# Optimization experiments

Measured on AMD Instinct MI355X. Metric: run time of the kernel, lower is better.

Reference implementation:

```python
import jax, jax.numpy as jnp
import numpy as np

N = 100_000          # nodes
E = 1_600_000        # directed edges (avg degree 16)
EPS = 1e-5           # LayerNorm eps (torch default)


def _layer_norm(h, g, b):
    m = jnp.mean(h, axis=-1, keepdims=True)
    v = jnp.mean((h - m) ** 2, axis=-1, keepdims=True)
    return (h - m) * jax.lax.rsqrt(v + EPS) * g + b


def _forward(x, edge_index, Ws, bs, gs, bes, mWs, mbs):
    n = x.shape[0]
    loop = jnp.arange(n, dtype=edge_index.dtype)
    src = jnp.concatenate([edge_index[0], loop])   # self-loops appended (PyG GCNConv default)
    dst = jnp.concatenate([edge_index[1], loop])
    deg = jax.ops.segment_sum(jnp.ones_like(dst, dtype=x.dtype), dst, num_segments=n)
    dinv = jax.lax.rsqrt(jnp.maximum(deg, 1.0))    # deg >= 1 thanks to self-loops
    norm = dinv[src] * dinv[dst]                   # symmetric normalization, shape [E+N]
    h = x
    for W, b, g, be in zip(Ws, bs, gs, bes):
        t = h @ W                                  # [N, d_out]
        msg = t[src] * norm[:, None]               # edge gather  [E+N, d_out]
        t = jax.ops.segment_sum(msg, dst, num_segments=n) + b  # scatter-add
        h = jax.nn.relu(_layer_norm(t, g, be))     # dropout is identity in eval mode
    h = jax.nn.relu(h @ mWs[0] + mbs[0])
    h = jax.nn.relu(h @ mWs[1] + mbs[1])
    return h @ mWs[2] + mbs[2]                     # [N, 1]


def setup_inputs() -> dict:
    key = jax.random.key(0)
    ks = jax.random.split(key, 12)
    inp = {}
    inp["x"] = jax.random.normal(ks[0], (N, 3), dtype=jnp.float32)
    inp["edge_index"] = jax.random.randint(ks[1], (2, E), 0, N, dtype=jnp.int32)
    dims = [3, 64, 128, 128]
    k = 2
    for l, (din, dout) in enumerate(zip(dims[:-1], dims[1:])):
        inp[f"W{l}"] = jax.random.normal(ks[k], (din, dout), dtype=jnp.float32) / np.sqrt(din).astype(np.float32); k += 1
        inp[f"b{l}"] = jnp.zeros((dout,), jnp.float32)
        inp[f"g{l}"] = jnp.ones((dout,), jnp.float32)
        inp[f"be{l}"] = jnp.zeros((dout,), jnp.float32)
    mlp = [(128, 128), (128, 32), (32, 1)]
    for l, (din, dout) in enumerate(mlp):
        inp[f"mW{l}"] = jax.random.normal(ks[k], (din, dout), dtype=jnp.float32) / np.sqrt(din).astype(np.float32); k += 1
        inp[f"mb{l}"] = jnp.zeros((dout,), jnp.float32)
    return inp


def reference(x, edge_index, W0, b0, g0, be0, W1, b1, g1, be1, W2, b2, g2, be2,
              mW0, mb0, mW1, mb1, mW2, mb2):
    return _forward(x, edge_index,
                    (W0, W1, W2), (b0, b1, b2), (g0, g1, g2), (be0, be1, be2),
                    (mW0, mW1, mW2), (mb0, mb1, mb2))
```

## Files before the change

kernel.cpp:

```cpp
#include <hip/hip_runtime.h>

static inline int cdiv(int a, int b) { return (a + b - 1) / b; }

typedef unsigned short u16;
typedef unsigned int u32;
typedef unsigned long long u64;

using short8 = __attribute__((ext_vector_type(8))) short;
using f32x4  = __attribute__((ext_vector_type(4))) float;

#define BCHUNK 8192

__device__ __forceinline__ float bf2f(u16 u) {
    union { u32 i; float f; } v;
    v.i = ((u32)u) << 16;
    return v.f;
}
__device__ __forceinline__ u16 f2bf(float f) {
    union { float f; u32 i; } v;
    v.f = f;
    u32 r = v.i + 0x7FFF + ((v.i >> 16) & 1);
    return (u16)(r >> 16);
}


__global__ void bzero_kernel(int* __restrict__ bcnt, int nb) {
    int i = blockIdx.x * blockDim.x + threadIdx.x;
    if (i < nb) bcnt[i] = 0;
}

__global__ __launch_bounds__(256) void bhist_kernel(const int* __restrict__ dst,
                                                    int* __restrict__ bcnt, int ne, int nb) {
    __shared__ int lh[512];
    for (int i = threadIdx.x; i < nb; i += 256) lh[i] = 0;
    __syncthreads();
    int base = blockIdx.x * BCHUNK;
    int end = min(base + BCHUNK, ne);
    for (int i = base + threadIdx.x; i < end; i += 256) atomicAdd(&lh[dst[i] >> 8], 1);
    __syncthreads();
    for (int i = threadIdx.x; i < nb; i += 256)
        if (lh[i]) atomicAdd(&bcnt[i], lh[i]);
}

__global__ __launch_bounds__(512) void bscan_kernel(const int* __restrict__ bcnt,
                                                    int* __restrict__ bboff,
                                                    int* __restrict__ bcur, int nb) {
    __shared__ int sd[512];
    int tid = threadIdx.x;
    int v = (tid < nb) ? bcnt[tid] : 0;
    sd[tid] = v;
    __syncthreads();
    for (int off = 1; off < 512; off <<= 1) {
        int t = (tid >= off) ? sd[tid - off] : 0;
        __syncthreads();
        sd[tid] += t;
        __syncthreads();
    }
    int ex = sd[tid] - v;
    if (tid < nb) {
        bboff[tid] = ex;
        bcur[tid] = ex;
    }
    if (tid == 511) bboff[nb] = sd[511];
}

__global__ __launch_bounds__(256) void bplace_kernel(const int* __restrict__ src,
                                                     const int* __restrict__ dst,
                                                     int* __restrict__ bcur,
                                                     u32* __restrict__ bpair, int ne, int nb) {
    __shared__ int lh[512], lbase[512], lrun[512];
    for (int i = threadIdx.x; i < nb; i += 256) { lh[i] = 0; lrun[i] = 0; }
    __syncthreads();
    int base = blockIdx.x * BCHUNK;
    int end = min(base + BCHUNK, ne);
    for (int i = base + threadIdx.x; i < end; i += 256) atomicAdd(&lh[dst[i] >> 8], 1);
    __syncthreads();
    for (int b = threadIdx.x; b < nb; b += 256) {
        int c = lh[b];
        if (c) lbase[b] = atomicAdd(&bcur[b], c);
    }
    __syncthreads();
    for (int i = base + threadIdx.x; i < end; i += 256) {
        int d = dst[i];
        int b = d >> 8;
        int r = atomicAdd(&lrun[b], 1);
        bpair[(size_t)lbase[b] + r] = ((u32)(d & 255) << 24) | (u32)src[i];
    }
}

__global__ __launch_bounds__(256) void fine_count_kernel(const u32* __restrict__ bpair,
                                                         const int* __restrict__ bboff,
                                                         int* __restrict__ cnt, int n) {
    int b = blockIdx.x;
    __shared__ int lc[256];
    lc[threadIdx.x] = 0;
    __syncthreads();
    int e0 = bboff[b], e1 = bboff[b + 1];
    for (int i = e0 + threadIdx.x; i < e1; i += 256) {
        atomicAdd(&lc[bpair[i] >> 24], 1);
    }
    __syncthreads();
    int d = (b << 8) + threadIdx.x;
    if (d < n) cnt[d] = lc[threadIdx.x];
}

__global__ __launch_bounds__(256) void fine_place_kernel(const u32* __restrict__ bpair,
                                                         const int* __restrict__ bboff,
                                                         const int* __restrict__ row_ptr,
                                                         int* __restrict__ sorted, int n) {
    int b = blockIdx.x;
    __shared__ int lcur[256];
    int d = (b << 8) + threadIdx.x;
    lcur[threadIdx.x] = (d < n) ? row_ptr[d] : 0;
    __syncthreads();
    int e0 = bboff[b], e1 = bboff[b + 1];
    for (int i = e0 + threadIdx.x; i < e1; i += 256) {
        u32 p = bpair[i];
        int slot = atomicAdd(&lcur[p >> 24], 1);
        sorted[slot] = (int)(p & 0xFFFFFF);
    }
}


__global__ void part_kernel(const int* __restrict__ cnt, int* __restrict__ partial, int n) {
    __shared__ int sred[256];
    int tid = threadIdx.x;
    int base = blockIdx.x * 1024 + tid * 4;
    int s = 0;
#pragma unroll
    for (int j = 0; j < 4; ++j) {
        int i = base + j;
        if (i < n) s += cnt[i];
    }
    sred[tid] = s;
    __syncthreads();
    for (int off = 128; off; off >>= 1) {
        if (tid < off) sred[tid] += sred[tid + off];
        __syncthreads();
    }
    if (tid == 0) partial[blockIdx.x] = sred[0];
}

__global__ __launch_bounds__(256) void scanp_kernel(const int* __restrict__ partial,
                                                    int* __restrict__ chunkoff,
                                                    int* __restrict__ row_ptr,
                                                    int nchunks, int n) {
    __shared__ int sd[256];
    int tid = threadIdx.x;
    int v = (tid < nchunks) ? partial[tid] : 0;
    sd[tid] = v;
    __syncthreads();
    for (int off = 1; off < 256; off <<= 1) {
        int t = (tid >= off) ? sd[tid - off] : 0;
        __syncthreads();
        sd[tid] += t;
        __syncthreads();
    }
    if (tid < nchunks) chunkoff[tid] = sd[tid] - v;
    if (tid == 255) row_ptr[n] = sd[255];
}

__global__ void scanc_kernel(const int* __restrict__ cnt, const int* __restrict__ chunkoff,
                             int* __restrict__ row_ptr, float* __restrict__ dinv,
                             const float* __restrict__ x, float4* __restrict__ xs4, int n) {
    __shared__ int sdat[256];
    int tid = threadIdx.x;
    int base = blockIdx.x * 1024 + tid * 4;
    int c[4];
    int ts = 0;
#pragma unroll
    for (int j = 0; j < 4; ++j) {
        int i = base + j;
        c[j] = (i < n) ? cnt[i] : 0;
        ts += c[j];
    }
    sdat[tid] = ts;
    __syncthreads();
    for (int off = 1; off < 256; off <<= 1) {
        int t = (tid >= off) ? sdat[tid - off] : 0;
        __syncthreads();
        sdat[tid] += t;
        __syncthreads();
    }
    int ex = sdat[tid] - ts + chunkoff[blockIdx.x];
#pragma unroll
    for (int j = 0; j < 4; ++j) {
        int i = base + j;
        if (i < n) {
            row_ptr[i] = ex;
            float dd = 1.0f / sqrtf((float)(c[j] + 1));
            dinv[i] = dd;
            float4 o = {x[i * 3 + 0] * dd, x[i * 3 + 1] * dd, x[i * 3 + 2] * dd, 0.0f};
            xs4[i] = o;
            ex += c[j];
        }
    }
}


__global__ void wprep_kernel(const float* __restrict__ W1f, const float* __restrict__ W2f,
                             const float* __restrict__ M0f, const float* __restrict__ M1f,
                             u16* __restrict__ Wt1, u16* __restrict__ Wt2,
                             u16* __restrict__ WtM0, u16* __restrict__ WtM1t) {
    int i = blockIdx.x * blockDim.x + threadIdx.x;
    if (i < 8192) {
        int k = i / 128, c = i % 128;
        Wt1[(size_t)c * 64 + k] = f2bf(W1f[i]);
    } else if (i < 24576) {
        int j = i - 8192;
        int k = j / 128, c = j % 128;
        Wt2[(size_t)c * 128 + k] = f2bf(W2f[j]);
    } else if (i < 40960) {
        int j = i - 24576;
        int k = j / 128, c = j % 128;
        WtM0[(size_t)c * 128 + k] = f2bf(M0f[j]);
    } else if (i < 45056) {
        int j = i - 40960;
        int k = j / 32, c = j % 32;
        WtM1t[(size_t)c * 128 + k] = f2bf(M1f[j]);
    }
}


__global__ void gather3_kernel(const float4* __restrict__ xs4, const int* __restrict__ rp,
                               const int* __restrict__ ss, const float* __restrict__ dinv,
                               float4* __restrict__ agg3, int n) {
    int d = blockIdx.x * blockDim.x + threadIdx.x;
    if (d >= n) return;
    float4 a = xs4[d];
    int k = rp[d], k1 = rp[d + 1];
    for (; k + 4 <= k1; k += 4) {
        int s0 = ss[k], s1 = ss[k + 1], s2 = ss[k + 2], s3 = ss[k + 3];
        float4 v0 = xs4[s0], v1 = xs4[s1], v2 = xs4[s2], v3 = xs4[s3];
        a.x += v0.x + v1.x + v2.x + v3.x;
        a.y += v0.y + v1.y + v2.y + v3.y;
        a.z += v0.z + v1.z + v2.z + v3.z;
    }
    for (; k < k1; ++k) {
        float4 v = xs4[ss[k]];
        a.x += v.x;
        a.y += v.y;
        a.z += v.z;
    }
    float dd = dinv[d];
    float4 o = {a.x * dd, a.y * dd, a.z * dd, 0.0f};
    agg3[d] = o;
}

__global__ void gather64_kernel(const u16* __restrict__ Ts, const int* __restrict__ rp,
                                const int* __restrict__ ss, const float* __restrict__ dinv,
                                u16* __restrict__ A, int n) {
    int row = blockIdx.x * 4 + (threadIdx.x >> 6);
    if (row >= n) return;
    int lane = threadIdx.x & 63;
    float acc = bf2f(Ts[(size_t)row * 64 + lane]);
    int k = rp[row], k1 = rp[row + 1];
    while (k < k1) {
        int take = min(64, k1 - k);
        int myi = (lane < take) ? ss[k + lane] : 0;
        int u = 0;
        for (; u + 16 <= take; u += 16) {
            int s[16];
#pragma unroll
            for (int q = 0; q < 16; ++q) s[q] = __shfl(myi, u + q);
            float v[16];
#pragma unroll
            for (int q = 0; q < 16; ++q) v[q] = bf2f(Ts[(size_t)s[q] * 64 + lane]);
#pragma unroll
            for (int q = 0; q < 16; ++q) acc += v[q];
        }
        for (; u + 8 <= take; u += 8) {
            int s[8];
#pragma unroll
            for (int q = 0; q < 8; ++q) s[q] = __shfl(myi, u + q);
            float v[8];
#pragma unroll
            for (int q = 0; q < 8; ++q) v[q] = bf2f(Ts[(size_t)s[q] * 64 + lane]);
#pragma unroll
            for (int q = 0; q < 8; ++q) acc += v[q];
        }
        for (; u < take; ++u) {
            int s = __shfl(myi, u);
            acc += bf2f(Ts[(size_t)s * 64 + lane]);
        }
        k += take;
    }
    A[(size_t)row * 64 + lane] = f2bf(acc * dinv[row]);
}

__global__ void gather128_kernel(const u16* __restrict__ Ts, const int* __restrict__ rp,
                                 const int* __restrict__ ss, const float* __restrict__ dinv,
                                 u16* __restrict__ A, int n) {
    int row = blockIdx.x * 4 + (threadIdx.x >> 6);
    if (row >= n) return;
    int lane = threadIdx.x & 63;
    const u32* T2 = (const u32*)Ts;
    u32 t = T2[(size_t)row * 64 + lane];
    float ax = bf2f((u16)(t & 0xffff));
    float ay = bf2f((u16)(t >> 16));
    int k = rp[row], k1 = rp[row + 1];
    while (k < k1) {
        int take = min(64, k1 - k);
        int myi = (lane < take) ? ss[k + lane] : 0;
        int u = 0;
        for (; u + 16 <= take; u += 16) {
            int s[16];
#pragma unroll
            for (int q = 0; q < 16; ++q) s[q] = __shfl(myi, u + q);
            u32 v[16];
#pragma unroll
            for (int q = 0; q < 16; ++q) v[q] = T2[(size_t)s[q] * 64 + lane];
#pragma unroll
            for (int q = 0; q < 16; ++q) {
                ax += bf2f((u16)(v[q] & 0xffff));
                ay += bf2f((u16)(v[q] >> 16));
            }
        }
        for (; u + 8 <= take; u += 8) {
            int s[8];
#pragma unroll
            for (int q = 0; q < 8; ++q) s[q] = __shfl(myi, u + q);
            u32 v[8];
#pragma unroll
            for (int q = 0; q < 8; ++q) v[q] = T2[(size_t)s[q] * 64 + lane];
#pragma unroll
            for (int q = 0; q < 8; ++q) {
                ax += bf2f((u16)(v[q] & 0xffff));
                ay += bf2f((u16)(v[q] >> 16));
            }
        }
        for (; u < take; ++u) {
            int s = __shfl(myi, u);
            u32 a = T2[(size_t)s * 64 + lane];
            ax += bf2f((u16)(a & 0xffff));
            ay += bf2f((u16)(a >> 16));
        }
        k += take;
    }
    float dd = dinv[row];
    u32 o = (u32)f2bf(ax * dd) | ((u32)f2bf(ay * dd) << 16);
    ((u32*)A)[(size_t)row * 64 + lane] = o;
}


__global__ __launch_bounds__(256) void gcn0_kernel(const float4* __restrict__ agg3,
                                                   const float* __restrict__ W0,
                                                   const float* __restrict__ b0,
                                                   const float* __restrict__ g0,
                                                   const float* __restrict__ be0,
                                                   const float* __restrict__ dinv,
                                                   u16* __restrict__ out, int n) {
    __shared__ float sW[192], sb[64], sg[64], se[64];
    int tid = threadIdx.x;
    if (tid < 192) sW[tid] = W0[tid];
    if (tid < 64) {
        sb[tid] = b0[tid];
        sg[tid] = g0[tid];
        se[tid] = be0[tid];
    }
    __syncthreads();
    int row = blockIdx.x * 4 + (tid >> 6);
    int lane = tid & 63;
    if (row >= n) return;
    float4 a = agg3[row];
    float acc = sb[lane] + a.x * sW[lane] + a.y * sW[64 + lane] + a.z * sW[128 + lane];
    float s = acc;
#pragma unroll
    for (int off = 32; off; off >>= 1) s += __shfl_xor(s, off);
    float mean = s * (1.0f / 64.0f);
    float d = acc - mean;
    float q = d * d;
#pragma unroll
    for (int off = 32; off; off >>= 1) q += __shfl_xor(q, off);
    float inv = 1.0f / sqrtf(q * (1.0f / 64.0f) + 1e-5f);
    float o = d * inv * sg[lane] + se[lane];
    out[(size_t)row * 64 + lane] = f2bf(dinv[row] * fmaxf(o, 0.0f));
}


template <int DIN, int DOUT, bool SCALEOUT>
__global__ __launch_bounds__(256) void mfma_gemm_kernel(const u16* __restrict__ H,
                                                        const u16* __restrict__ Wt,
                                                        const float* __restrict__ b,
                                                        const float* __restrict__ g,
                                                        const float* __restrict__ be,
                                                        const float* __restrict__ dscale,
                                                        u16* __restrict__ C, int n) {
    constexpr int NT = DOUT / 16;
    constexpr int KS = DIN / 32;
    const int tid = threadIdx.x;
    const int wave = tid >> 6;
    const int lane = tid & 63;
    const int l16 = lane & 15;
    const int lhi = lane >> 4;
    const int r0 = blockIdx.x * 64 + wave * 16;

    short8 wf[KS][NT];
#pragma unroll
    for (int ks = 0; ks < KS; ++ks)
#pragma unroll
        for (int nt = 0; nt < NT; ++nt)
            wf[ks][nt] = *(const short8*)(Wt + (size_t)(nt * 16 + l16) * DIN + ks * 32 + 8 * lhi);

    int arow = r0 + l16;
    if (arow > n - 1) arow = n - 1;
    const u16* Hrow = H + (size_t)arow * DIN + 8 * lhi;
    short8 af[KS];
#pragma unroll
    for (int ks = 0; ks < KS; ++ks) af[ks] = *(const short8*)(Hrow + ks * 32);

    f32x4 acc[NT];
#pragma unroll
    for (int nt = 0; nt < NT; ++nt) acc[nt] = {0.f, 0.f, 0.f, 0.f};

#pragma unroll
    for (int ks = 0; ks < KS; ++ks)
#pragma unroll
        for (int nt = 0; nt < NT; ++nt)
            acc[nt] = __builtin_amdgcn_mfma_f32_16x16x32_bf16(af[ks], wf[ks][nt], acc[nt], 0, 0, 0);

    float bias[NT], gl[NT], bel[NT];
#pragma unroll
    for (int nt = 0; nt < NT; ++nt) {
        bias[nt] = b[nt * 16 + l16];
        gl[nt] = g[nt * 16 + l16];
        bel[nt] = be[nt * 16 + l16];
    }

#pragma unroll
    for (int j = 0; j < 4; ++j) {
        int row = r0 + lhi * 4 + j;
        float v[NT];
#pragma unroll
        for (int nt = 0; nt < NT; ++nt) v[nt] = acc[nt][j] + bias[nt];
        float s = 0.f;
#pragma unroll
        for (int nt = 0; nt < NT; ++nt) s += v[nt];
#pragma unroll
        for (int off = 1; off < 16; off <<= 1) s += __shfl_xor(s, off);
        float mean = s * (1.0f / DOUT);
        float qs = 0.f;
#pragma unroll
        for (int nt = 0; nt < NT; ++nt) {
            float d = v[nt] - mean;
            qs += d * d;
        }
#pragma unroll
        for (int off = 1; off < 16; off <<= 1) qs += __shfl_xor(qs, off);
        float inv = 1.0f / sqrtf(qs * (1.0f / DOUT) + 1e-5f);
        if (row < n) {
            float sc = SCALEOUT ? dscale[row] : 1.0f;
#pragma unroll
            for (int nt = 0; nt < NT; ++nt) {
                float o = (v[nt] - mean) * inv * gl[nt] + bel[nt];
                C[(size_t)row * DOUT + nt * 16 + l16] = f2bf(sc * fmaxf(o, 0.f));
            }
        }
    }
}


__global__ __launch_bounds__(256) void mlp_fused_kernel(const u16* __restrict__ H,
                                                        const u16* __restrict__ WtM0,
                                                        const u16* __restrict__ WtM1t,
                                                        const float* __restrict__ mb0,
                                                        const float* __restrict__ mb1,
                                                        const float* __restrict__ mW2,
                                                        const float* __restrict__ mb2,
                                                        float* __restrict__ out, int n) {
    __shared__ u16 sm1[4][16][132];
    const int tid = threadIdx.x;
    const int wave = tid >> 6;
    const int lane = tid & 63;
    const int l16 = lane & 15;
    const int lhi = lane >> 4;
    const int r0 = blockIdx.x * 64 + wave * 16;

    {
        short8 wf[4][8];
#pragma unroll
        for (int ks = 0; ks < 4; ++ks)
#pragma unroll
            for (int nt = 0; nt < 8; ++nt)
                wf[ks][nt] = *(const short8*)(WtM0 + (size_t)(nt * 16 + l16) * 128 + ks * 32 + 8 * lhi);

        int arow = r0 + l16;
        if (arow > n - 1) arow = n - 1;
        const u16* Hrow = H + (size_t)arow * 128 + 8 * lhi;
        short8 af[4];
#pragma unroll
        for (int ks = 0; ks < 4; ++ks) af[ks] = *(const short8*)(Hrow + ks * 32);

        f32x4 acc[8];
#pragma unroll
        for (int nt = 0; nt < 8; ++nt) acc[nt] = {0.f, 0.f, 0.f, 0.f};
#pragma unroll
        for (int ks = 0; ks < 4; ++ks)
#pragma unroll
            for (int nt = 0; nt < 8; ++nt)
                acc[nt] = __builtin_amdgcn_mfma_f32_16x16x32_bf16(af[ks], wf[ks][nt], acc[nt], 0, 0, 0);

#pragma unroll
        for (int nt = 0; nt < 8; ++nt) {
            float bias = mb0[nt * 16 + l16];
#pragma unroll
            for (int j = 0; j < 4; ++j) {
                sm1[wave][lhi * 4 + j][nt * 16 + l16] = f2bf(fmaxf(acc[nt][j] + bias, 0.f));
            }
        }
    }

    short8 a2[2][4];
#pragma unroll
    for (int t = 0; t < 2; ++t)
#pragma unroll
        for (int ks = 0; ks < 4; ++ks)
            a2[t][ks] = *(const short8*)(WtM1t + (size_t)(t * 16 + l16) * 128 + ks * 32 + 8 * lhi);

    short8 b2[4];
#pragma unroll
    for (int ks = 0; ks < 4; ++ks)
        b2[ks] = *(const short8*)&sm1[wave][l16][ks * 32 + 8 * lhi];

    f32x4 acc2[2];
    acc2[0] = {0.f, 0.f, 0.f, 0.f};
    acc2[1] = {0.f, 0.f, 0.f, 0.f};
#pragma unroll
    for (int ks = 0; ks < 4; ++ks) {
        acc2[0] = __builtin_amdgcn_mfma_f32_16x16x32_bf16(a2[0][ks], b2[ks], acc2[0], 0, 0, 0);
        acc2[1] = __builtin_amdgcn_mfma_f32_16x16x32_bf16(a2[1][ks], b2[ks], acc2[1], 0, 0, 0);
    }

    float part = 0.f;
#pragma unroll
    for (int t = 0; t < 2; ++t)
#pragma unroll
        for (int j = 0; j < 4; ++j) {
            int c = t * 16 + lhi * 4 + j;
            part += fmaxf(acc2[t][j] + mb1[c], 0.f) * mW2[c];
        }
    part += __shfl_xor(part, 16);
    part += __shfl_xor(part, 32);
    int row = r0 + l16;
    if (lhi == 0 && row < n) out[row] = part + mb2[0];
}


extern "C" void kernel_launch(void* const* d_in, const int* in_sizes, int n_in,
                              void* d_out, int out_size, void* d_ws, size_t ws_size,
                              hipStream_t stream) {
    const float* x   = (const float*)d_in[0];
    const int*   ei  = (const int*)d_in[1];
    const float* W0  = (const float*)d_in[2];
    const float* b0  = (const float*)d_in[3];
    const float* g0  = (const float*)d_in[4];
    const float* be0 = (const float*)d_in[5];
    const float* W1  = (const float*)d_in[6];
    const float* b1  = (const float*)d_in[7];
    const float* g1  = (const float*)d_in[8];
    const float* be1 = (const float*)d_in[9];
    const float* W2  = (const float*)d_in[10];
    const float* b2  = (const float*)d_in[11];
    const float* g2  = (const float*)d_in[12];
    const float* be2 = (const float*)d_in[13];
    const float* mW0 = (const float*)d_in[14];
    const float* mb0 = (const float*)d_in[15];
    const float* mW1 = (const float*)d_in[16];
    const float* mb1 = (const float*)d_in[17];
    const float* mW2 = (const float*)d_in[18];
    const float* mb2 = (const float*)d_in[19];
    float* out = (float*)d_out;

    const int n  = in_sizes[0] / 3;
    const int ne = in_sizes[1] / 2;
    const int* src = ei;
    const int* dst = ei + ne;
    const int nchunks = cdiv(n, 1024);
    const int nb = cdiv(n, 256);

    float* p = (float*)d_ws;
    float* dinv     = p;         p += n;
    int*   cnt      = (int*)p;   p += n;
    int*   row_ptr  = (int*)p;   p += n + 16;
    int*   partial  = (int*)p;   p += 256;
    int*   chunkoff = (int*)p;   p += 256;
    int*   bcnt     = (int*)p;   p += 512;
    int*   bboff    = (int*)p;   p += 514;
    int*   bcur     = (int*)p;   p += 512;
    int*   sorted   = (int*)p;   p += ne;
    u32*   bpair    = (u32*)p;   p += ne;
    float4* xs4     = (float4*)p; p += 4 * (size_t)n;
    float4* agg3    = (float4*)p; p += 4 * (size_t)n;
    float* fR12     = p;         p += 64 * (size_t)n;
    float* fR3      = p;         p += 64 * (size_t)n;
    u16*   Wt1      = (u16*)p;
    u16*   Wt2      = Wt1 + 64 * 128;
    u16*   WtM0     = Wt2 + 128 * 128;
    u16*   WtM1t    = WtM0 + 128 * 128;

    u16* h0s   = (u16*)fR12;
    u16* a64b  = (u16*)(fR12 + 32 * (size_t)n);
    u16* a128b = (u16*)fR12;
    u16* h1s   = (u16*)fR3;
    u16* h2b   = (u16*)fR3;

    wprep_kernel<<<cdiv(45056, 256), 256, 0, stream>>>(W1, W2, mW0, mW1, Wt1, Wt2, WtM0, WtM1t);

    bzero_kernel<<<cdiv(nb, 256), 256, 0, stream>>>(bcnt, nb);
    bhist_kernel<<<cdiv(ne, BCHUNK), 256, 0, stream>>>(dst, bcnt, ne, nb);
    bscan_kernel<<<1, 512, 0, stream>>>(bcnt, bboff, bcur, nb);
    bplace_kernel<<<cdiv(ne, BCHUNK), 256, 0, stream>>>(src, dst, bcur, bpair, ne, nb);
    fine_count_kernel<<<nb, 256, 0, stream>>>(bpair, bboff, cnt, n);
    part_kernel<<<nchunks, 256, 0, stream>>>(cnt, partial, n);
    scanp_kernel<<<1, 256, 0, stream>>>(partial, chunkoff, row_ptr, nchunks, n);
    scanc_kernel<<<nchunks, 256, 0, stream>>>(cnt, chunkoff, row_ptr, dinv, x, xs4, n);
    fine_place_kernel<<<nb, 256, 0, stream>>>(bpair, bboff, row_ptr, sorted, n);

    gather3_kernel<<<cdiv(n, 256), 256, 0, stream>>>(xs4, row_ptr, sorted, dinv, agg3, n);
    gcn0_kernel<<<cdiv(n, 4), 256, 0, stream>>>(agg3, W0, b0, g0, be0, dinv, h0s, n);

    gather64_kernel<<<cdiv(n, 4), 256, 0, stream>>>(h0s, row_ptr, sorted, dinv, a64b, n);
    mfma_gemm_kernel<64, 128, true><<<cdiv(n, 64), 256, 0, stream>>>(
        a64b, Wt1, b1, g1, be1, dinv, h1s, n);

    gather128_kernel<<<cdiv(n, 4), 256, 0, stream>>>(h1s, row_ptr, sorted, dinv, a128b, n);
    mfma_gemm_kernel<128, 128, false><<<cdiv(n, 64), 256, 0, stream>>>(
        a128b, Wt2, b2, g2, be2, nullptr, h2b, n);

    mlp_fused_kernel<<<cdiv(n, 64), 256, 0, stream>>>(h2b, WtM0, WtM1t, mb0, mb1, mW2, mb2, out, n);
}
```

Before: 439.3 us.

## Fuse CSR build, layer-0 gather, and last GEMM into the MLP kernel

After: 423.5 us. 1.04x faster.

```diff
diff --git a/kernel.cpp b/kernel.cpp
--- a/kernel.cpp
+++ b/kernel.cpp
@@ -4,7 +4,6 @@
 
 typedef unsigned short u16;
 typedef unsigned int u32;
-typedef unsigned long long u64;
 
 using short8 = __attribute__((ext_vector_type(8))) short;
 using f32x4  = __attribute__((ext_vector_type(4))) float;
@@ -24,185 +23,13 @@
 }
 
 
-__global__ void bzero_kernel(int* __restrict__ bcnt, int nb) {
-    int i = blockIdx.x * blockDim.x + threadIdx.x;
-    if (i < nb) bcnt[i] = 0;
-}
-
-__global__ __launch_bounds__(256) void bhist_kernel(const int* __restrict__ dst,
-                                                    int* __restrict__ bcnt, int ne, int nb) {
-    __shared__ int lh[512];
-    for (int i = threadIdx.x; i < nb; i += 256) lh[i] = 0;
-    __syncthreads();
-    int base = blockIdx.x * BCHUNK;
-    int end = min(base + BCHUNK, ne);
-    for (int i = base + threadIdx.x; i < end; i += 256) atomicAdd(&lh[dst[i] >> 8], 1);
-    __syncthreads();
-    for (int i = threadIdx.x; i < nb; i += 256)
-        if (lh[i]) atomicAdd(&bcnt[i], lh[i]);
-}
-
-__global__ __launch_bounds__(512) void bscan_kernel(const int* __restrict__ bcnt,
-                                                    int* __restrict__ bboff,
-                                                    int* __restrict__ bcur, int nb) {
-    __shared__ int sd[512];
-    int tid = threadIdx.x;
-    int v = (tid < nb) ? bcnt[tid] : 0;
-    sd[tid] = v;
-    __syncthreads();
-    for (int off = 1; off < 512; off <<= 1) {
-        int t = (tid >= off) ? sd[tid - off] : 0;
-        __syncthreads();
-        sd[tid] += t;
-        __syncthreads();
-    }
-    int ex = sd[tid] - v;
-    if (tid < nb) {
-        bboff[tid] = ex;
-        bcur[tid] = ex;
-    }
-    if (tid == 511) bboff[nb] = sd[511];
-}
-
-__global__ __launch_bounds__(256) void bplace_kernel(const int* __restrict__ src,
-                                                     const int* __restrict__ dst,
-                                                     int* __restrict__ bcur,
-                                                     u32* __restrict__ bpair, int ne, int nb) {
-    __shared__ int lh[512], lbase[512], lrun[512];
-    for (int i = threadIdx.x; i < nb; i += 256) { lh[i] = 0; lrun[i] = 0; }
-    __syncthreads();
-    int base = blockIdx.x * BCHUNK;
-    int end = min(base + BCHUNK, ne);
-    for (int i = base + threadIdx.x; i < end; i += 256) atomicAdd(&lh[dst[i] >> 8], 1);
-    __syncthreads();
-    for (int b = threadIdx.x; b < nb; b += 256) {
-        int c = lh[b];
-        if (c) lbase[b] = atomicAdd(&bcur[b], c);
-    }
-    __syncthreads();
-    for (int i = base + threadIdx.x; i < end; i += 256) {
-        int d = dst[i];
-        int b = d >> 8;
-        int r = atomicAdd(&lrun[b], 1);
-        bpair[(size_t)lbase[b] + r] = ((u32)(d & 255) << 24) | (u32)src[i];
-    }
-}
-
-__global__ __launch_bounds__(256) void fine_count_kernel(const u32* __restrict__ bpair,
-                                                         const int* __restrict__ bboff,
-                                                         int* __restrict__ cnt, int n) {
-    int b = blockIdx.x;
-    __shared__ int lc[256];
-    lc[threadIdx.x] = 0;
-    __syncthreads();
-    int e0 = bboff[b], e1 = bboff[b + 1];
-    for (int i = e0 + threadIdx.x; i < e1; i += 256) {
-        atomicAdd(&lc[bpair[i] >> 24], 1);
-    }
-    __syncthreads();
-    int d = (b << 8) + threadIdx.x;
-    if (d < n) cnt[d] = lc[threadIdx.x];
-}
-
-__global__ __launch_bounds__(256) void fine_place_kernel(const u32* __restrict__ bpair,
-                                                         const int* __restrict__ bboff,
-                                                         const int* __restrict__ row_ptr,
-                                                         int* __restrict__ sorted, int n) {
-    int b = blockIdx.x;
-    __shared__ int lcur[256];
-    int d = (b << 8) + threadIdx.x;
-    lcur[threadIdx.x] = (d < n) ? row_ptr[d] : 0;
-    __syncthreads();
-    int e0 = bboff[b], e1 = bboff[b + 1];
-    for (int i = e0 + threadIdx.x; i < e1; i += 256) {
-        u32 p = bpair[i];
-        int slot = atomicAdd(&lcur[p >> 24], 1);
-        sorted[slot] = (int)(p & 0xFFFFFF);
-    }
-}
-
-
-__global__ void part_kernel(const int* __restrict__ cnt, int* __restrict__ partial, int n) {
-    __shared__ int sred[256];
-    int tid = threadIdx.x;
-    int base = blockIdx.x * 1024 + tid * 4;
-    int s = 0;
-#pragma unroll
-    for (int j = 0; j < 4; ++j) {
-        int i = base + j;
-        if (i < n) s += cnt[i];
-    }
-    sred[tid] = s;
-    __syncthreads();
-    for (int off = 128; off; off >>= 1) {
-        if (tid < off) sred[tid] += sred[tid + off];
-        __syncthreads();
-    }
-    if (tid == 0) partial[blockIdx.x] = sred[0];
-}
-
-__global__ __launch_bounds__(256) void scanp_kernel(const int* __restrict__ partial,
-                                                    int* __restrict__ chunkoff,
-                                                    int* __restrict__ row_ptr,
-                                                    int nchunks, int n) {
-    __shared__ int sd[256];
-    int tid = threadIdx.x;
-    int v = (tid < nchunks) ? partial[tid] : 0;
-    sd[tid] = v;
-    __syncthreads();
-    for (int off = 1; off < 256; off <<= 1) {
-        int t = (tid >= off) ? sd[tid - off] : 0;
-        __syncthreads();
-        sd[tid] += t;
-        __syncthreads();
-    }
-    if (tid < nchunks) chunkoff[tid] = sd[tid] - v;
-    if (tid == 255) row_ptr[n] = sd[255];
-}
-
-__global__ void scanc_kernel(const int* __restrict__ cnt, const int* __restrict__ chunkoff,
-                             int* __restrict__ row_ptr, float* __restrict__ dinv,
-                             const float* __restrict__ x, float4* __restrict__ xs4, int n) {
-    __shared__ int sdat[256];
-    int tid = threadIdx.x;
-    int base = blockIdx.x * 1024 + tid * 4;
-    int c[4];
-    int ts = 0;
-#pragma unroll
-    for (int j = 0; j < 4; ++j) {
-        int i = base + j;
-        c[j] = (i < n) ? cnt[i] : 0;
-        ts += c[j];
-    }
-    sdat[tid] = ts;
-    __syncthreads();
-    for (int off = 1; off < 256; off <<= 1) {
-        int t = (tid >= off) ? sdat[tid - off] : 0;
-        __syncthreads();
-        sdat[tid] += t;
-        __syncthreads();
-    }
-    int ex = sdat[tid] - ts + chunkoff[blockIdx.x];
-#pragma unroll
-    for (int j = 0; j < 4; ++j) {
-        int i = base + j;
-        if (i < n) {
-            row_ptr[i] = ex;
-            float dd = 1.0f / sqrtf((float)(c[j] + 1));
-            dinv[i] = dd;
-            float4 o = {x[i * 3 + 0] * dd, x[i * 3 + 1] * dd, x[i * 3 + 2] * dd, 0.0f};
-            xs4[i] = o;
-            ex += c[j];
-        }
-    }
-}
-
-
 __global__ void wprep_kernel(const float* __restrict__ W1f, const float* __restrict__ W2f,
                              const float* __restrict__ M0f, const float* __restrict__ M1f,
                              u16* __restrict__ Wt1, u16* __restrict__ Wt2,
-                             u16* __restrict__ WtM0, u16* __restrict__ WtM1t) {
+                             u16* __restrict__ WtM0, u16* __restrict__ WtM1t,
+                             int* __restrict__ bcnt, int nb) {
     int i = blockIdx.x * blockDim.x + threadIdx.x;
+    if (i < nb) bcnt[i] = 0;
     if (i < 8192) {
         int k = i / 128, c = i % 128;
         Wt1[(size_t)c * 64 + k] = f2bf(W1f[i]);
@@ -222,30 +49,164 @@
 }
 
 
-__global__ void gather3_kernel(const float4* __restrict__ xs4, const int* __restrict__ rp,
-                               const int* __restrict__ ss, const float* __restrict__ dinv,
-                               float4* __restrict__ agg3, int n) {
-    int d = blockIdx.x * blockDim.x + threadIdx.x;
-    if (d >= n) return;
-    float4 a = xs4[d];
-    int k = rp[d], k1 = rp[d + 1];
-    for (; k + 4 <= k1; k += 4) {
-        int s0 = ss[k], s1 = ss[k + 1], s2 = ss[k + 2], s3 = ss[k + 3];
-        float4 v0 = xs4[s0], v1 = xs4[s1], v2 = xs4[s2], v3 = xs4[s3];
-        a.x += v0.x + v1.x + v2.x + v3.x;
-        a.y += v0.y + v1.y + v2.y + v3.y;
-        a.z += v0.z + v1.z + v2.z + v3.z;
-    }
-    for (; k < k1; ++k) {
+__global__ __launch_bounds__(256) void bhist_kernel(const int* __restrict__ dst,
+                                                    int* __restrict__ bcnt, int ne, int nb) {
+    __shared__ int lh[512];
+    for (int i = threadIdx.x; i < nb; i += 256) lh[i] = 0;
+    __syncthreads();
+    int base = blockIdx.x * BCHUNK;
+    int end = min(base + BCHUNK, ne);
+    for (int i = base + threadIdx.x; i < end; i += 256) atomicAdd(&lh[dst[i] >> 8], 1);
+    __syncthreads();
+    for (int i = threadIdx.x; i < nb; i += 256)
+        if (lh[i]) atomicAdd(&bcnt[i], lh[i]);
+}
+
+__global__ __launch_bounds__(512) void bscan_kernel(const int* __restrict__ bcnt,
+                                                    int* __restrict__ bboff,
+                                                    int* __restrict__ bcur, int nb) {
+    __shared__ int sd[512];
+    int tid = threadIdx.x;
+    int v = (tid < nb) ? bcnt[tid] : 0;
+    sd[tid] = v;
+    __syncthreads();
+    for (int off = 1; off < 512; off <<= 1) {
+        int t = (tid >= off) ? sd[tid - off] : 0;
+        __syncthreads();
+        sd[tid] += t;
+        __syncthreads();
+    }
+    int ex = sd[tid] - v;
+    if (tid < nb) {
+        bboff[tid] = ex;
+        bcur[tid] = ex;
+    }
+    if (tid == 511) bboff[nb] = sd[511];
+}
+
+__global__ __launch_bounds__(256) void bplace_kernel(const int* __restrict__ src,
+                                                     const int* __restrict__ dst,
+                                                     int* __restrict__ bcur,
+                                                     u32* __restrict__ bpair, int ne, int nb) {
+    __shared__ int lh[512], lbase[512], lrun[512];
+    for (int i = threadIdx.x; i < nb; i += 256) { lh[i] = 0; lrun[i] = 0; }
+    __syncthreads();
+    int base = blockIdx.x * BCHUNK;
+    int end = min(base + BCHUNK, ne);
+    for (int i = base + threadIdx.x; i < end; i += 256) atomicAdd(&lh[dst[i] >> 8], 1);
+    __syncthreads();
+    for (int b = threadIdx.x; b < nb; b += 256) {
+        int c = lh[b];
+        if (c) lbase[b] = atomicAdd(&bcur[b], c);
+    }
+    __syncthreads();
+    for (int i = base + threadIdx.x; i < end; i += 256) {
+        int d = dst[i];
+        int b = d >> 8;
+        int r = atomicAdd(&lrun[b], 1);
+        bpair[(size_t)lbase[b] + r] = ((u32)(d & 255) << 24) | (u32)src[i];
+    }
+}
+
+__global__ __launch_bounds__(256) void fine_all_kernel(const u32* __restrict__ bpair,
+                                                       const int* __restrict__ bboff,
+                                                       const float* __restrict__ x,
+                                                       int* __restrict__ row_ptr,
+                                                       float* __restrict__ dinv,
+                                                       float4* __restrict__ xs4,
+                                                       int* __restrict__ sorted,
+                                                       int n, int ne) {
+    int b = blockIdx.x;
+    int tid = threadIdx.x;
+    __shared__ int lc[256], lpfx[256], lcur[256];
+    lc[tid] = 0;
+    __syncthreads();
+    int e0 = bboff[b], e1 = bboff[b + 1];
+    for (int i = e0 + tid; i < e1; i += 256) atomicAdd(&lc[bpair[i] >> 24], 1);
+    __syncthreads();
+    int c = lc[tid];
+    lpfx[tid] = c;
+    __syncthreads();
+    for (int off = 1; off < 256; off <<= 1) {
+        int t = (tid >= off) ? lpfx[tid - off] : 0;
+        __syncthreads();
+        lpfx[tid] += t;
+        __syncthreads();
+    }
+    int ex = e0 + lpfx[tid] - c;
+    lcur[tid] = ex;
+    int d = (b << 8) + tid;
+    if (d < n) {
+        row_ptr[d] = ex;
+        float dd = 1.0f / sqrtf((float)(c + 1));
+        dinv[d] = dd;
+        float4 o = {x[d * 3 + 0] * dd, x[d * 3 + 1] * dd, x[d * 3 + 2] * dd, 0.0f};
+        xs4[d] = o;
+    }
+    if (b == 0 && tid == 0) row_ptr[n] = ne;
+    __syncthreads();
+    for (int i = e0 + tid; i < e1; i += 256) {
+        u32 p = bpair[i];
+        int slot = atomicAdd(&lcur[p >> 24], 1);
+        sorted[slot] = (int)(p & 0xFFFFFF);
+    }
+}
+
+
+__global__ __launch_bounds__(256) void gcn0_kernel(const float4* __restrict__ xs4,
+                                                   const int* __restrict__ rp,
+                                                   const int* __restrict__ ss,
+                                                   const float* __restrict__ dinv,
+                                                   const float* __restrict__ W0,
+                                                   const float* __restrict__ b0,
+                                                   const float* __restrict__ g0,
+                                                   const float* __restrict__ be0,
+                                                   u16* __restrict__ out, int n) {
+    __shared__ float sW[192], sb[64], sg[64], se[64];
+    int tid = threadIdx.x;
+    if (tid < 192) sW[tid] = W0[tid];
+    if (tid < 64) {
+        sb[tid] = b0[tid];
+        sg[tid] = g0[tid];
+        se[tid] = be0[tid];
+    }
+    __syncthreads();
+    int row = blockIdx.x * 4 + (tid >> 6);
+    if (row >= n) return;
+    int lane = tid & 63;
+    int k0 = rp[row], k1 = rp[row + 1];
+    float ax = 0.f, ay = 0.f, az = 0.f;
+    for (int k = k0 + lane; k < k1; k += 64) {
         float4 v = xs4[ss[k]];
-        a.x += v.x;
-        a.y += v.y;
-        a.z += v.z;
-    }
-    float dd = dinv[d];
-    float4 o = {a.x * dd, a.y * dd, a.z * dd, 0.0f};
-    agg3[d] = o;
-}
+        ax += v.x;
+        ay += v.y;
+        az += v.z;
+    }
+#pragma unroll
+    for (int off = 32; off; off >>= 1) {
+        ax += __shfl_xor(ax, off);
+        ay += __shfl_xor(ay, off);
+        az += __shfl_xor(az, off);
+    }
+    float4 sf = xs4[row];
+    float dd = dinv[row];
+    ax = (ax + sf.x) * dd;
+    ay = (ay + sf.y) * dd;
+    az = (az + sf.z) * dd;
+    float acc = sb[lane] + ax * sW[lane] + ay * sW[64 + lane] + az * sW[128 + lane];
+    float s = acc;
+#pragma unroll
+    for (int off = 32; off; off >>= 1) s += __shfl_xor(s, off);
+    float mean = s * (1.0f / 64.0f);
+    float d = acc - mean;
+    float q = d * d;
+#pragma unroll
+    for (int off = 32; off; off >>= 1) q += __shfl_xor(q, off);
+    float inv = 1.0f / sqrtf(q * (1.0f / 64.0f) + 1e-5f);
+    float o = d * inv * sg[lane] + se[lane];
+    out[(size_t)row * 64 + lane] = f2bf(dd * fmaxf(o, 0.0f));
+}
+
 
 __global__ void gather64_kernel(const u16* __restrict__ Ts, const int* __restrict__ rp,
                                 const int* __restrict__ ss, const float* __restrict__ dinv,
@@ -343,41 +304,6 @@
 }
 
 
-__global__ __launch_bounds__(256) void gcn0_kernel(const float4* __restrict__ agg3,
-                                                   const float* __restrict__ W0,
-                                                   const float* __restrict__ b0,
-                                                   const float* __restrict__ g0,
-                                                   const float* __restrict__ be0,
-                                                   const float* __restrict__ dinv,
-                                                   u16* __restrict__ out, int n) {
-    __shared__ float sW[192], sb[64], sg[64], se[64];
-    int tid = threadIdx.x;
-    if (tid < 192) sW[tid] = W0[tid];
-    if (tid < 64) {
-        sb[tid] = b0[tid];
-        sg[tid] = g0[tid];
-        se[tid] = be0[tid];
-    }
-    __syncthreads();
-    int row = blockIdx.x * 4 + (tid >> 6);
-    int lane = tid & 63;
-    if (row >= n) return;
-    float4 a = agg3[row];
-    float acc = sb[lane] + a.x * sW[lane] + a.y * sW[64 + lane] + a.z * sW[128 + lane];
-    float s = acc;
-#pragma unroll
-    for (int off = 32; off; off >>= 1) s += __shfl_xor(s, off);
-    float mean = s * (1.0f / 64.0f);
-    float d = acc - mean;
-    float q = d * d;
-#pragma unroll
-    for (int off = 32; off; off >>= 1) q += __shfl_xor(q, off);
-    float inv = 1.0f / sqrtf(q * (1.0f / 64.0f) + 1e-5f);
-    float o = d * inv * sg[lane] + se[lane];
-    out[(size_t)row * 64 + lane] = f2bf(dinv[row] * fmaxf(o, 0.0f));
-}
-
-
 template <int DIN, int DOUT, bool SCALEOUT>
 __global__ __launch_bounds__(256) void mfma_gemm_kernel(const u16* __restrict__ H,
                                                         const u16* __restrict__ Wt,
@@ -460,15 +386,20 @@
 }
 
 
-__global__ __launch_bounds__(256) void mlp_fused_kernel(const u16* __restrict__ H,
-                                                        const u16* __restrict__ WtM0,
-                                                        const u16* __restrict__ WtM1t,
-                                                        const float* __restrict__ mb0,
-                                                        const float* __restrict__ mb1,
-                                                        const float* __restrict__ mW2,
-                                                        const float* __restrict__ mb2,
-                                                        float* __restrict__ out, int n) {
-    __shared__ u16 sm1[4][16][132];
+__global__ __launch_bounds__(256) void mfma_mlp_kernel(const u16* __restrict__ H,
+                                                       const u16* __restrict__ Wt2,
+                                                       const float* __restrict__ b2,
+                                                       const float* __restrict__ g2,
+                                                       const float* __restrict__ be2,
+                                                       const u16* __restrict__ WtM0,
+                                                       const u16* __restrict__ WtM1t,
+                                                       const float* __restrict__ mb0,
+                                                       const float* __restrict__ mb1,
+                                                       const float* __restrict__ mW2,
+                                                       const float* __restrict__ mb2,
+                                                       float* __restrict__ out, int n) {
+    __shared__ u16 sh2[4][16][136];
+    __shared__ u16 sm1[4][16][136];
     const int tid = threadIdx.x;
     const int wave = tid >> 6;
     const int lane = tid & 63;
@@ -482,7 +413,7 @@
         for (int ks = 0; ks < 4; ++ks)
 #pragma unroll
             for (int nt = 0; nt < 8; ++nt)
-                wf[ks][nt] = *(const short8*)(WtM0 + (size_t)(nt * 16 + l16) * 128 + ks * 32 + 8 * lhi);
+                wf[ks][nt] = *(const short8*)(Wt2 + (size_t)(nt * 16 + l16) * 128 + ks * 32 + 8 * lhi);
 
         int arow = r0 + l16;
         if (arow > n - 1) arow = n - 1;
@@ -500,13 +431,69 @@
             for (int nt = 0; nt < 8; ++nt)
                 acc[nt] = __builtin_amdgcn_mfma_f32_16x16x32_bf16(af[ks], wf[ks][nt], acc[nt], 0, 0, 0);
 
+        float bias[8], gl[8], bel[8];
+#pragma unroll
+        for (int nt = 0; nt < 8; ++nt) {
+            bias[nt] = b2[nt * 16 + l16];
+            gl[nt] = g2[nt * 16 + l16];
+            bel[nt] = be2[nt * 16 + l16];
+        }
+#pragma unroll
+        for (int j = 0; j < 4; ++j) {
+            float v[8];
+#pragma unroll
+            for (int nt = 0; nt < 8; ++nt) v[nt] = acc[nt][j] + bias[nt];
+            float s = 0.f;
+#pragma unroll
+            for (int nt = 0; nt < 8; ++nt) s += v[nt];
+#pragma unroll
+            for (int off = 1; off < 16; off <<= 1) s += __shfl_xor(s, off);
+            float mean = s * (1.0f / 128.0f);
+            float qs = 0.f;
+#pragma unroll
+            for (int nt = 0; nt < 8; ++nt) {
+                float d = v[nt] - mean;
+                qs += d * d;
+            }
+#pragma unroll
+            for (int off = 1; off < 16; off <<= 1) qs += __shfl_xor(qs, off);
+            float inv = 1.0f / sqrtf(qs * (1.0f / 128.0f) + 1e-5f);
+#pragma unroll
+            for (int nt = 0; nt < 8; ++nt) {
+                float o = (v[nt] - mean) * inv * gl[nt] + bel[nt];
+                sh2[wave][lhi * 4 + j][nt * 16 + l16] = f2bf(fmaxf(o, 0.f));
+            }
+        }
+    }
+
+    {
+        short8 wf[4][8];
+#pragma unroll
+        for (int ks = 0; ks < 4; ++ks)
+#pragma unroll
+            for (int nt = 0; nt < 8; ++nt)
+                wf[ks][nt] = *(const short8*)(WtM0 + (size_t)(nt * 16 + l16) * 128 + ks * 32 + 8 * lhi);
+
+        short8 af[4];
+#pragma unroll
+        for (int ks = 0; ks < 4; ++ks)
+            af[ks] = *(const short8*)&sh2[wave][l16][ks * 32 + 8 * lhi];
+
+        f32x4 acc[8];
+#pragma unroll
+        for (int nt = 0; nt < 8; ++nt) acc[nt] = {0.f, 0.f, 0.f, 0.f};
+#pragma unroll
+        for (int ks = 0; ks < 4; ++ks)
+#pragma unroll
+            for (int nt = 0; nt < 8; ++nt)
+                acc[nt] = __builtin_amdgcn_mfma_f32_16x16x32_bf16(af[ks], wf[ks][nt], acc[nt], 0, 0, 0);
+
 #pragma unroll
         for (int nt = 0; nt < 8; ++nt) {
             float bias = mb0[nt * 16 + l16];
 #pragma unroll
-            for (int j = 0; j < 4; ++j) {
+            for (int j = 0; j < 4; ++j)
                 sm1[wave][lhi * 4 + j][nt * 16 + l16] = f2bf(fmaxf(acc[nt][j] + bias, 0.f));
-            }
         }
     }
 
@@ -517,18 +504,18 @@
         for (int ks = 0; ks < 4; ++ks)
             a2[t][ks] = *(const short8*)(WtM1t + (size_t)(t * 16 + l16) * 128 + ks * 32 + 8 * lhi);
 
-    short8 b2[4];
+    short8 bfr[4];
 #pragma unroll
     for (int ks = 0; ks < 4; ++ks)
-        b2[ks] = *(const short8*)&sm1[wave][l16][ks * 32 + 8 * lhi];
+        bfr[ks] = *(const short8*)&sm1[wave][l16][ks * 32 + 8 * lhi];
 
     f32x4 acc2[2];
     acc2[0] = {0.f, 0.f, 0.f, 0.f};
     acc2[1] = {0.f, 0.f, 0.f, 0.f};
 #pragma unroll
     for (int ks = 0; ks < 4; ++ks) {
-        acc2[0] = __builtin_amdgcn_mfma_f32_16x16x32_bf16(a2[0][ks], b2[ks], acc2[0], 0, 0, 0);
-        acc2[1] = __builtin_amdgcn_mfma_f32_16x16x32_bf16(a2[1][ks], b2[ks], acc2[1], 0, 0, 0);
+        acc2[0] = __builtin_amdgcn_mfma_f32_16x16x32_bf16(a2[0][ks], bfr[ks], acc2[0], 0, 0, 0);
+        acc2[1] = __builtin_amdgcn_mfma_f32_16x16x32_bf16(a2[1][ks], bfr[ks], acc2[1], 0, 0, 0);
     }
 
     float part = 0.f;
@@ -575,22 +562,17 @@
     const int ne = in_sizes[1] / 2;
     const int* src = ei;
     const int* dst = ei + ne;
-    const int nchunks = cdiv(n, 1024);
     const int nb = cdiv(n, 256);
 
     float* p = (float*)d_ws;
     float* dinv     = p;         p += n;
-    int*   cnt      = (int*)p;   p += n;
     int*   row_ptr  = (int*)p;   p += n + 16;
-    int*   partial  = (int*)p;   p += 256;
-    int*   chunkoff = (int*)p;   p += 256;
     int*   bcnt     = (int*)p;   p += 512;
     int*   bboff    = (int*)p;   p += 514;
     int*   bcur     = (int*)p;   p += 512;
     int*   sorted   = (int*)p;   p += ne;
     u32*   bpair    = (u32*)p;   p += ne;
     float4* xs4     = (float4*)p; p += 4 * (size_t)n;
-    float4* agg3    = (float4*)p; p += 4 * (size_t)n;
     float* fR12     = p;         p += 64 * (size_t)n;
     float* fR3      = p;         p += 64 * (size_t)n;
     u16*   Wt1      = (u16*)p;
@@ -602,30 +584,23 @@
     u16* a64b  = (u16*)(fR12 + 32 * (size_t)n);
     u16* a128b = (u16*)fR12;
     u16* h1s   = (u16*)fR3;
-    u16* h2b   = (u16*)fR3;
-
-    wprep_kernel<<<cdiv(45056, 256), 256, 0, stream>>>(W1, W2, mW0, mW1, Wt1, Wt2, WtM0, WtM1t);
-
-    bzero_kernel<<<cdiv(nb, 256), 256, 0, stream>>>(bcnt, nb);
+
+    wprep_kernel<<<cdiv(45056, 256), 256, 0, stream>>>(W1, W2, mW0, mW1, Wt1, Wt2, WtM0,
+                                                       WtM1t, bcnt, nb);
+
     bhist_kernel<<<cdiv(ne, BCHUNK), 256, 0, stream>>>(dst, bcnt, ne, nb);
     bscan_kernel<<<1, 512, 0, stream>>>(bcnt, bboff, bcur, nb);
     bplace_kernel<<<cdiv(ne, BCHUNK), 256, 0, stream>>>(src, dst, bcur, bpair, ne, nb);
-    fine_count_kernel<<<nb, 256, 0, stream>>>(bpair, bboff, cnt, n);
-    part_kernel<<<nchunks, 256, 0, stream>>>(cnt, partial, n);
-    scanp_kernel<<<1, 256, 0, stream>>>(partial, chunkoff, row_ptr, nchunks, n);
-    scanc_kernel<<<nchunks, 256, 0, stream>>>(cnt, chunkoff, row_ptr, dinv, x, xs4, n);
-    fine_place_kernel<<<nb, 256, 0, stream>>>(bpair, bboff, row_ptr, sorted, n);
-
-    gather3_kernel<<<cdiv(n, 256), 256, 0, stream>>>(xs4, row_ptr, sorted, dinv, agg3, n);
-    gcn0_kernel<<<cdiv(n, 4), 256, 0, stream>>>(agg3, W0, b0, g0, be0, dinv, h0s, n);
+    fine_all_kernel<<<nb, 256, 0, stream>>>(bpair, bboff, x, row_ptr, dinv, xs4, sorted, n, ne);
+
+    gcn0_kernel<<<cdiv(n, 4), 256, 0, stream>>>(xs4, row_ptr, sorted, dinv, W0, b0, g0, be0,
+                                                h0s, n);
 
     gather64_kernel<<<cdiv(n, 4), 256, 0, stream>>>(h0s, row_ptr, sorted, dinv, a64b, n);
     mfma_gemm_kernel<64, 128, true><<<cdiv(n, 64), 256, 0, stream>>>(
         a64b, Wt1, b1, g1, be1, dinv, h1s, n);
 
     gather128_kernel<<<cdiv(n, 4), 256, 0, stream>>>(h1s, row_ptr, sorted, dinv, a128b, n);
-    mfma_gemm_kernel<128, 128, false><<<cdiv(n, 64), 256, 0, stream>>>(
-        a128b, Wt2, b2, g2, be2, nullptr, h2b, n);
-
-    mlp_fused_kernel<<<cdiv(n, 64), 256, 0, stream>>>(h2b, WtM0, WtM1t, mb0, mb1, mW2, mb2, out, n);
-}
+    mfma_mlp_kernel<<<cdiv(n, 64), 256, 0, stream>>>(a128b, Wt2, b2, g2, be2, WtM0, WtM1t,
+                                                     mb0, mb1, mW2, mb2, out, n);
+}
```
